# Kernel tuning notes

Measured on AMD Instinct MI355X. Metric: run time of the kernel, lower is better.

## Reference

```python
import jax, jax.numpy as jnp
import numpy as np

# JetBlock dims
B, T, HID = 2, 2048, 2048
H, DK, DV = 16, 128, 128
W = 4                      # dynamic short-conv kernel size
GEN_IN = 2 * H * DK        # kernel generator conditioned on concat(q, k)
GEN_HID = H * DV
EPS_NORM = 1e-6
EPS_L2 = 1e-12


def _silu(x):
    return x * jax.nn.sigmoid(x)


def setup_inputs() -> dict:
    key = jax.random.key(0)
    ks = jax.random.split(key, 12)
    s = 0.02
    return {
        "x": jax.random.normal(ks[0], (B, T, HID), jnp.float32),
        "Wq": jax.random.normal(ks[1], (HID, H * DK), jnp.float32) * s,
        "Wk": jax.random.normal(ks[2], (HID, H * DK), jnp.float32) * s,
        "Wv": jax.random.normal(ks[3], (HID, H * DV), jnp.float32) * s,
        "Wb": jax.random.normal(ks[4], (HID, H), jnp.float32) * s,
        "Wa": jax.random.normal(ks[5], (HID, H), jnp.float32) * s,
        "dt_bias": jax.random.normal(ks[6], (H,), jnp.float32) * s,
        "A_log": jax.random.normal(ks[7], (H,), jnp.float32) * 0.5,
        "gen_w1": jax.random.normal(ks[8], (GEN_IN, GEN_HID), jnp.float32) * s,
        "gen_w2": jax.random.normal(ks[9], (GEN_HID, H * DV * W), jnp.float32) * s,
        "gen_b2": jnp.zeros((H * DV * W,), jnp.float32),
        "norm_weight": jnp.ones((DV,), jnp.float32),
        "Wg": jax.random.normal(ks[10], (HID, H * DV), jnp.float32) * s,
        "Wo": jax.random.normal(ks[11], (H * DV, HID), jnp.float32) * s,
    }


def reference(x, Wq, Wk, Wv, Wb, Wa, dt_bias, A_log, gen_w1, gen_w2, gen_b2,
              norm_weight, Wg, Wo):
    # projections
    q = (x @ Wq).reshape(B, T, H, DK)
    k = (x @ Wk).reshape(B, T, H, DK)
    v = x @ Wv  # [B, T, H*DV]

    # dynamic short convolution on v, kernels generated from concat(q, k)
    gi = jnp.concatenate([q.reshape(B, T, -1), k.reshape(B, T, -1)], axis=-1)
    kern = (_silu(gi @ gen_w1) @ gen_w2 + gen_b2).reshape(B, T, H * DV, W)
    vp = jnp.pad(v, ((0, 0), (W - 1, 0), (0, 0)))  # causal left pad
    # out[t, d] = sum_w kern[t, d, w] * v[t - (W-1) + w, d]
    vconv = kern[..., 0] * vp[:, 0:T, :]
    for w in range(1, W):
        vconv = vconv + kern[..., w] * vp[:, w:w + T, :]
    v = _silu(vconv).reshape(B, T, H, DV)

    # gating params (gated-deltanet parameterization)
    beta = jax.nn.sigmoid(x @ Wb)                              # [B, T, H]
    g = -jnp.exp(A_log) * jax.nn.softplus(x @ Wa + dt_bias)    # log-space decay <= 0
    decay = jnp.exp(g)

    # qk l2 norm (F.normalize semantics)
    qn = q / jnp.maximum(jnp.linalg.norm(q, axis=-1, keepdims=True), EPS_L2)
    kn = k / jnp.maximum(jnp.linalg.norm(k, axis=-1, keepdims=True), EPS_L2)

    # gated delta rule recurrence (o_t reads state BEFORE the update, per source)
    def step(S, inps):
        q_t, k_t, v_t, g_t, b_t = inps
        o_t = jnp.einsum('bnkv,bnk->bnv', S, q_t)
        Sk = jnp.einsum('bnkv,bnk->bnv', S, k_t)
        delta = v_t - Sk
        S = g_t[..., None, None] * S + b_t[..., None, None] * (
            k_t[..., :, None] * delta[..., None, :])
        return S, o_t

    S0 = jnp.zeros((B, H, DK, DV), x.dtype)
    xs = (jnp.moveaxis(qn, 1, 0), jnp.moveaxis(kn, 1, 0), jnp.moveaxis(v, 1, 0),
          jnp.moveaxis(decay, 1, 0), jnp.moveaxis(beta, 1, 0))
    _, o = jax.lax.scan(step, S0, xs)           # o: [T, B, H, DV]
    o = jnp.moveaxis(o, 0, 1)                   # [B, T, H, DV]

    # gated RMSNorm per head, then output projection
    gate = (x @ Wg).reshape(B, T, H, DV)
    rms = o * jax.lax.rsqrt(jnp.mean(o * o, axis=-1, keepdims=True) + EPS_NORM)
    o = rms * norm_weight * _silu(gate)
    return o.reshape(B, T, H * DV) @ Wo
```

## Files before the change

kernel.cpp:

```cpp
#include <hip/hip_runtime.h>
#include <hip/hip_bf16.h>


typedef _Float16 v8h __attribute__((ext_vector_type(8)));
typedef _Float16 v4h __attribute__((ext_vector_type(4)));
typedef _Float16 v2h __attribute__((ext_vector_type(2)));
typedef float    v4f __attribute__((ext_vector_type(4)));

__device__ __forceinline__ void gload16(const void* g, void* l) {
  __builtin_amdgcn_global_load_lds(
      (const __attribute__((address_space(1))) unsigned int*)g,
      (__attribute__((address_space(3))) unsigned int*)l, 16, 0, 0);
}

__global__ __launch_bounds__(256)
void transpose_cast(const float* __restrict__ src, _Float16* __restrict__ dst,
                    int R, int C)
{
  __shared__ float tile[32][33];
  int c0 = blockIdx.x * 32, r0 = blockIdx.y * 32;
  int tx = threadIdx.x & 31, ty = threadIdx.x >> 5;
  #pragma unroll
  for (int i = 0; i < 32; i += 8)
    tile[ty + i][tx] = src[(size_t)(r0 + ty + i) * C + c0 + tx];
  __syncthreads();
  #pragma unroll
  for (int i = 0; i < 32; i += 8)
    dst[(size_t)(c0 + ty + i) * R + r0 + tx] = (_Float16)tile[tx][ty + i];
}

__global__ __launch_bounds__(256)
void cast_f32_f16(const float* __restrict__ src, _Float16* __restrict__ dst, int n4)
{
  int i = blockIdx.x * 256 + threadIdx.x;
  if (i >= n4) return;
  float4 v = ((const float4*)src)[i];
  v4h h = {(_Float16)v.x, (_Float16)v.y, (_Float16)v.z, (_Float16)v.w};
  *(v4h*)&dst[4 * (size_t)i] = h;
}

template<int MODE>
__global__ __launch_bounds__(512, 2)
void gemm256(const _Float16* __restrict__ A, const _Float16* __restrict__ Bt,
             void* __restrict__ Cout, const float* __restrict__ bias,
             int M, int N, int K)
{
  __shared__ _Float16 lds[65536];
  const int tid  = threadIdx.x;
  const int lane = tid & 63;
  const int wid  = tid >> 6;
  const int wm   = wid >> 2;
  const int wn   = wid & 3;
  const int l16  = lane & 15;
  const int q8   = (lane >> 4) * 8;
  const int swzx = (l16 & 7) << 3;

  const int nbx = N >> 8;
  const int cpx = gridDim.x >> 3;
  const int swz = (blockIdx.x & 7) * cpx + (blockIdx.x >> 3);
  const int bm0 = (swz / nbx) << 8;
  const int bn0 = (swz % nbx) << 8;

  const _Float16* Abase = A  + (size_t)bm0 * K;
  const _Float16* Bbase = Bt + (size_t)bn0 * K;

  const int r0 = tid >> 3;
  const int cs = ((tid & 7) * 8) ^ ((r0 & 7) << 3);

#define SLOTA(par, half) (lds + ((par) * 2 + (half)) * 8192)
#define SLOTB(par, half) (lds + 32768 + ((par) * 2 + (half)) * 8192)
#define STAGE(basep, kt, slot) do {                                        \
    _Float16* sst_ = (slot);                                               \
    gload16((basep) + (size_t)r0 * K + (kt) + cs, sst_ + tid * 8);         \
    gload16((basep) + (size_t)(r0 + 64) * K + (kt) + cs,                   \
            sst_ + 4096 + tid * 8);                                        \
  } while (0)
#define LOADA(par, mh) do {                                                \
    const _Float16* sld_ = SLOTA(par, mh);                                 \
    _Pragma("unroll")                                                      \
    for (int ks = 0; ks < 2; ks++)                                         \
      _Pragma("unroll")                                                    \
      for (int mi = 0; mi < 4; mi++)                                       \
        af[ks][mi] = *(const v8h*)&sld_[(wm * 64 + mi * 16 + l16) * 64 +   \
                                        ((ks * 32 + q8) ^ swzx)];          \
  } while (0)
#define LOADB(par, nh) do {                                                \
    const _Float16* sld_ = SLOTB(par, nh);                                 \
    _Pragma("unroll")                                                      \
    for (int ks = 0; ks < 2; ks++)                                         \
      _Pragma("unroll")                                                    \
      for (int ni = 0; ni < 2; ni++)                                       \
        bf[ks][ni] = *(const v8h*)&sld_[(wn * 32 + ni * 16 + l16) * 64 +   \
                                        ((ks * 32 + q8) ^ swzx)];          \
  } while (0)
#define MMAC(mh, nh) do {                                                  \
    __builtin_amdgcn_s_setprio(1);                                         \
    _Pragma("unroll")                                                      \
    for (int ks = 0; ks < 2; ks++)                                         \
      _Pragma("unroll")                                                    \
      for (int mi = 0; mi < 4; mi++)                                       \
        _Pragma("unroll")                                                  \
        for (int ni = 0; ni < 2; ni++)                                     \
          acc[mh][mi][nh][ni] = __builtin_amdgcn_mfma_f32_16x16x32_f16(    \
              af[ks][mi], bf[ks][ni], acc[mh][mi][nh][ni], 0, 0, 0);       \
    __builtin_amdgcn_s_setprio(0);                                         \
  } while (0)

  v4f acc[2][4][2][2];
  #pragma unroll
  for (int mh = 0; mh < 2; mh++)
    #pragma unroll
    for (int mi = 0; mi < 4; mi++)
      #pragma unroll
      for (int nh = 0; nh < 2; nh++)
        #pragma unroll
        for (int ni = 0; ni < 2; ni++)
          acc[mh][mi][nh][ni] = v4f{0.f, 0.f, 0.f, 0.f};
  v8h af[2][4], bf[2][2];

  const int nt = K >> 6;

  STAGE(Abase,                   0,  SLOTA(0, 0));
  STAGE(Bbase,                   0,  SLOTB(0, 0));
  STAGE(Abase + (size_t)128 * K, 0,  SLOTA(0, 1));
  STAGE(Bbase + (size_t)128 * K, 0,  SLOTB(0, 1));
  STAGE(Abase,                   64, SLOTA(1, 0));
  STAGE(Bbase + (size_t)128 * K, 64, SLOTB(1, 1));
  asm volatile("s_waitcnt vmcnt(4)" ::: "memory");
  __builtin_amdgcn_s_barrier();

  for (int T = 0; T < nt; T++) {
    const int par = T & 1;
    const int kt1 = (T + 1) << 6;
    const int kt2 = (T + 2) << 6;
    LOADA(par, 0);
    LOADB(par, 0);
    if (T + 1 < nt) STAGE(Abase + (size_t)128 * K, kt1, SLOTA(par ^ 1, 1));
    __builtin_amdgcn_s_barrier();
    MMAC(0, 0);
    __builtin_amdgcn_s_barrier();
    LOADB(par, 1);
    if (T + 1 < nt) STAGE(Bbase, kt1, SLOTB(par ^ 1, 0));
    __builtin_amdgcn_s_barrier();
    MMAC(0, 1);
    __builtin_amdgcn_s_barrier();
    LOADA(par, 1);
    if (T + 2 < nt) STAGE(Abase, kt2, SLOTA(par, 0));
    __builtin_amdgcn_s_barrier();
    MMAC(1, 1);
    __builtin_amdgcn_s_barrier();
    LOADB(par, 0);
    if (T + 2 < nt) STAGE(Bbase + (size_t)128 * K, kt2, SLOTB(par, 1));
    __builtin_amdgcn_s_barrier();
    MMAC(1, 0);
    if (T + 2 < nt) { asm volatile("s_waitcnt vmcnt(4)" ::: "memory"); }
    else            { asm volatile("s_waitcnt vmcnt(0)" ::: "memory"); }
    __builtin_amdgcn_s_barrier();
  }

  const int q4 = (lane >> 4) * 4;
  #pragma unroll
  for (int mh = 0; mh < 2; mh++) {
    #pragma unroll
    for (int mi = 0; mi < 4; mi++) {
      #pragma unroll
      for (int nh = 0; nh < 2; nh++) {
        #pragma unroll
        for (int ni = 0; ni < 2; ni++) {
          const int gn = bn0 + nh * 128 + wn * 32 + ni * 16 + l16;
          #pragma unroll
          for (int r = 0; r < 4; r++) {
            const int gm = bm0 + mh * 128 + wm * 64 + mi * 16 + q4 + r;
            float val = acc[mh][mi][nh][ni][r];
            size_t offc = (size_t)gm * N + gn;
            if (MODE == 0) {
              ((float*)Cout)[offc] = val;
            } else if (MODE == 1) {
              float s = val / (1.0f + expf(-val));
              ((_Float16*)Cout)[offc] = (_Float16)s;
            } else if (MODE == 2) {
              float s = val + bias[gn];
              ((_Float16*)Cout)[offc] = (_Float16)s;
            } else {
              ((_Float16*)Cout)[offc] = (_Float16)val;
            }
          }
        }
      }
    }
  }
#undef SLOTA
#undef SLOTB
#undef STAGE
#undef LOADA
#undef LOADB
#undef MMAC
}

__global__ __launch_bounds__(256)
void conv_silu(const _Float16* __restrict__ vg, const _Float16* __restrict__ kernc,
               float* __restrict__ vprime, int chunk)
{
  int idx = blockIdx.x * 256 + threadIdx.x;
  int btl = idx >> 11;
  int d   = idx & 2047;
  int btg = chunk * 2048 + btl;
  v4h kv = *(const v4h*)&kernc[(size_t)btl * 8192 + d * 4];
  float kw0 = (float)kv[0], kw1 = (float)kv[1], kw2 = (float)kv[2], kw3 = (float)kv[3];
  const _Float16* vcol = vg + d;
  float acc = kw3 * (float)vcol[(size_t)btg * 4096];
  if (btl >= 1) acc += kw2 * (float)vcol[(size_t)(btg - 1) * 4096];
  if (btl >= 2) acc += kw1 * (float)vcol[(size_t)(btg - 2) * 4096];
  if (btl >= 3) acc += kw0 * (float)vcol[(size_t)(btg - 3) * 4096];
  vprime[(size_t)btg * 2048 + d] = acc / (1.0f + expf(-acc));
}

__global__ __launch_bounds__(256)
void beta_decay(const float* __restrict__ x, const float* __restrict__ Wb,
                const float* __restrict__ Wa, const float* __restrict__ dt_bias,
                const float* __restrict__ A_log,
                float* __restrict__ beta, float* __restrict__ glog)
{
  __shared__ float xs[2048];
  __shared__ float red[8][32];
  int row = blockIdx.x;
  int tid = threadIdx.x;
  for (int i = tid; i < 2048; i += 256) xs[i] = x[(size_t)row * 2048 + i];
  __syncthreads();
  int j = tid & 31, kg = tid >> 5;
  const float* W = (j < 16) ? Wb : Wa;
  int jj = j & 15;
  float acc = 0.f;
  int k0 = kg * 256;
  for (int k = k0; k < k0 + 256; k++) acc += xs[k] * W[(size_t)k * 16 + jj];
  red[kg][j] = acc;
  __syncthreads();
  if (tid < 32) {
    float s = 0.f;
    #pragma unroll
    for (int g2 = 0; g2 < 8; g2++) s += red[g2][tid];
    int hh = tid & 15;
    if (tid < 16) {
      beta[(size_t)row * 16 + hh] = 1.0f / (1.0f + expf(-s));
    } else {
      float tt = s + dt_bias[hh];
      float sp = (tt > 20.f) ? tt : log1pf(expf(tt));
      glog[(size_t)row * 16 + hh] = -expf(A_log[hh]) * sp;
    }
  }
}

__global__ __launch_bounds__(256)
void recurrence_chunked(const _Float16* __restrict__ gi,
                        const float* __restrict__ vprime,
                        const float* __restrict__ betab,
                        const float* __restrict__ glogb,
                        float* __restrict__ o)
{
  __shared__ _Float16 Q16[32][136];
  __shared__ _Float16 K16[32][136];
  __shared__ _Float16 KT16[2][128][40];
  __shared__ _Float16 St16[64][136];
  __shared__ float V32[32][68];
  __shared__ float W0L[32][65];
  __shared__ float O0L[32][65];
  __shared__ float At32[32][32];
  __shared__ _Float16 B16[32][40];
  __shared__ _Float16 Ut16[64][40];
  __shared__ _Float16 Utp16[64][40];
  __shared__ float lgA[2][32], lgm1A[2][32], gm1E[2][32], bGA[2][32],
                   psA[2][32], betA[2][32], p31A[2];

  const int tid  = threadIdx.x;
  const int wid  = tid >> 6;
  const int lane = tid & 63;
  const int l16  = lane & 15;
  const int q8   = (lane >> 4) * 8;
  const int q4   = (lane >> 4) * 4;
  const int rg   = lane >> 4;
  const int wc   = wid * 16 + l16;

  const int blk = blockIdx.x;
  const int dvh = blk & 1;
  const int h   = (blk >> 1) & 15;
  const int b   = blk >> 5;

  const _Float16* gq = gi + (size_t)b * 2048 * 4096 + h * 128;
  const _Float16* gk = gq + 2048;
  const float* vsrc = vprime + (size_t)b * 2048 * 2048 + h * 128 + dvh * 64;
  float* ob = o + ((size_t)b * 2048 * 16 + h) * 128 + dvh * 64;

  const int sr  = tid >> 3;
  const int sc8 = tid & 7;
  const int c0  = sc8 * 16;

  v4f sfr[8];
  #pragma unroll
  for (int tn = 0; tn < 8; tn++) sfr[tn] = v4f{0.f, 0.f, 0.f, 0.f};

  v8h pq0, pq1, pk0, pk1;
  float4 pv0, pv1;
  float pg = 0.f, pb = 0.f;

  auto stage_regs = [&](int t0) {
    pq0 = *(const v8h*)(gq + (size_t)(t0 + sr) * 4096 + c0);
    pq1 = *(const v8h*)(gq + (size_t)(t0 + sr) * 4096 + c0 + 8);
    pk0 = *(const v8h*)(gk + (size_t)(t0 + sr) * 4096 + c0);
    pk1 = *(const v8h*)(gk + (size_t)(t0 + sr) * 4096 + c0 + 8);
    pv0 = *(const float4*)(vsrc + (size_t)(t0 + sr) * 2048 + sc8 * 8);
    pv1 = *(const float4*)(vsrc + (size_t)(t0 + sr) * 2048 + sc8 * 8 + 4);
    if (tid < 32) {
      size_t bt_ = (size_t)(b * 2048 + t0 + tid) * 16 + h;
      pg = glogb[bt_];
      pb = betab[bt_];
    }
  };

  auto write_stage = [&](int pn) {
    float qf[16], kf[16];
    #pragma unroll
    for (int m = 0; m < 8; m++) {
      qf[m] = (float)pq0[m]; qf[m + 8] = (float)pq1[m];
      kf[m] = (float)pk0[m]; kf[m + 8] = (float)pk1[m];
    }
    float ssq = 0.f, ssk = 0.f;
    #pragma unroll
    for (int m = 0; m < 16; m++) { ssq += qf[m] * qf[m]; ssk += kf[m] * kf[m]; }
    ssq += __shfl_xor(ssq, 1); ssq += __shfl_xor(ssq, 2); ssq += __shfl_xor(ssq, 4);
    ssk += __shfl_xor(ssk, 1); ssk += __shfl_xor(ssk, 2); ssk += __shfl_xor(ssk, 4);
    float iq = 1.0f / fmaxf(sqrtf(ssq), 1e-12f);
    float ik = 1.0f / fmaxf(sqrtf(ssk), 1e-12f);
    v8h qo0, qo1, ko0, ko1;
    #pragma unroll
    for (int m = 0; m < 8; m++) {
      qo0[m] = (_Float16)(qf[m] * iq); qo1[m] = (_Float16)(qf[m + 8] * iq);
      ko0[m] = (_Float16)(kf[m] * ik); ko1[m] = (_Float16)(kf[m + 8] * ik);
    }
    *(v8h*)&Q16[sr][c0]     = qo0;
    *(v8h*)&Q16[sr][c0 + 8] = qo1;
    *(v8h*)&K16[sr][c0]     = ko0;
    *(v8h*)&K16[sr][c0 + 8] = ko1;
    #pragma unroll
    for (int m = 0; m < 8; m++) {
      KT16[pn][c0 + m][sr]     = ko0[m];
      KT16[pn][c0 + 8 + m][sr] = ko1[m];
    }
    *(float4*)&V32[sr][sc8 * 8]     = pv0;
    *(float4*)&V32[sr][sc8 * 8 + 4] = pv1;
    if (tid < 32) {
      float s = pg;
      #pragma unroll
      for (int d = 1; d < 32; d <<= 1) {
        float t = __shfl_up(s, d, 64);
        if (lane >= d) s += t;
      }
      float lg31 = __shfl(s, 31, 64);
      float lgm1 = s - pg;
      lgA[pn][lane]   = s;
      lgm1A[pn][lane] = lgm1;
      float g1 = expf(lgm1);
      gm1E[pn][lane]  = g1;
      bGA[pn][lane]   = pb * g1;
      psA[pn][lane]   = expf(lg31 - s);
      betA[pn][lane]  = pb;
      if (lane == 0) p31A[pn] = expf(lg31);
    }
  };

  stage_regs(0);
  for (int i = tid; i < 64 * 136; i += 256) (&St16[0][0])[i] = (_Float16)0.f;
  write_stage(0);
  __syncthreads();

  const v4f zf = {0.f, 0.f, 0.f, 0.f};

  for (int c = 0; c < 64; c++) {
    const int par = c & 1;

    if (c < 63) { stage_regs((c + 1) * 32); __builtin_amdgcn_sched_barrier(0); }

    v4f kkf = zf, qkf = zf, w0f0 = zf, w0f1 = zf, o0f0 = zf, o0f1 = zf;
    {
      const int ai = (wid >> 1) * 16 + l16;
      const int bj = (wid & 1) * 16 + l16;
      #pragma unroll
      for (int ks = 0; ks < 4; ks++) {
        const int ko = ks * 32 + q8;
        v8h bs  = *(const v8h*)&St16[wid * 16 + l16][ko];
        v8h ak0 = *(const v8h*)&K16[l16][ko];
        v8h ak1 = *(const v8h*)&K16[16 + l16][ko];
        v8h aq0 = *(const v8h*)&Q16[l16][ko];
        v8h aq1 = *(const v8h*)&Q16[16 + l16][ko];
        w0f0 = __builtin_amdgcn_mfma_f32_16x16x32_f16(ak0, bs, w0f0, 0, 0, 0);
        w0f1 = __builtin_amdgcn_mfma_f32_16x16x32_f16(ak1, bs, w0f1, 0, 0, 0);
        o0f0 = __builtin_amdgcn_mfma_f32_16x16x32_f16(aq0, bs, o0f0, 0, 0, 0);
        o0f1 = __builtin_amdgcn_mfma_f32_16x16x32_f16(aq1, bs, o0f1, 0, 0, 0);
        v8h akk = *(const v8h*)&K16[ai][ko];
        v8h aqq = *(const v8h*)&Q16[ai][ko];
        v8h bkk = *(const v8h*)&K16[bj][ko];
        kkf = __builtin_amdgcn_mfma_f32_16x16x32_f16(akk, bkk, kkf, 0, 0, 0);
        qkf = __builtin_amdgcn_mfma_f32_16x16x32_f16(aqq, bkk, qkf, 0, 0, 0);
      }
    }
    {
      const int i0 = (wid >> 1) * 16, j = (wid & 1) * 16 + l16;
      #pragma unroll
      for (int fr = 0; fr < 4; fr++) {
        const int i = i0 + q4 + fr;
        float ex = expf(fminf(lgm1A[par][i] - lgA[par][j], 0.f));
        const bool lt = (j < i);
        At32[j][i] = lt ? betA[par][i] * ex * kkf[fr] : 0.f;
        B16[i][j]  = lt ? (_Float16)(ex * qkf[fr]) : (_Float16)0.f;
      }
      #pragma unroll
      for (int fr = 0; fr < 4; fr++) {
        W0L[q4 + fr][wid * 16 + l16]      = w0f0[fr];
        W0L[16 + q4 + fr][wid * 16 + l16] = w0f1[fr];
        O0L[q4 + fr][wid * 16 + l16]      = o0f0[fr];
        O0L[16 + q4 + fr][wid * 16 + l16] = o0f1[fr];
      }
    }
    __syncthreads();

    float ru[8];
    #pragma unroll
    for (int jj = 0; jj < 8; jj++) {
      const int row = rg * 8 + jj;
      ru[jj] = betA[par][row] * V32[row][wc] - bGA[par][row] * W0L[row][wc];
    }
    #pragma unroll
    for (int j = 0; j < 32; j++) {
      float uj = __shfl(ru[j & 7], (j >> 3) * 16 + l16, 64);
      const v4f a0 = *(const v4f*)&At32[j][rg * 8];
      const v4f a1 = *(const v4f*)&At32[j][rg * 8 + 4];
      ru[0] -= a0[0] * uj; ru[1] -= a0[1] * uj;
      ru[2] -= a0[2] * uj; ru[3] -= a0[3] * uj;
      ru[4] -= a1[0] * uj; ru[5] -= a1[1] * uj;
      ru[6] -= a1[2] * uj; ru[7] -= a1[3] * uj;
    }
    {
      v8h uo, upo;
      #pragma unroll
      for (int jj = 0; jj < 8; jj++) {
        uo[jj]  = (_Float16)ru[jj];
        upo[jj] = (_Float16)(ru[jj] * psA[par][rg * 8 + jj]);
      }
      *(v8h*)&Ut16[wc][rg * 8]  = uo;
      *(v8h*)&Utp16[wc][rg * 8] = upo;
    }
    __syncthreads();

    {
      v8h bu = *(const v8h*)&Ut16[wid * 16 + l16][q8];
      #pragma unroll
      for (int t2i = 0; t2i < 2; t2i++) {
        v8h a = *(const v8h*)&B16[t2i * 16 + l16][q8];
        v4f d = __builtin_amdgcn_mfma_f32_16x16x32_f16(a, bu, zf, 0, 0, 0);
        #pragma unroll
        for (int fr = 0; fr < 4; fr++) {
          const int i = t2i * 16 + q4 + fr;
          const int cc = wid * 16 + l16;
          ob[(size_t)(c * 32 + i) * 2048 + cc] =
              gm1E[par][i] * O0L[i][cc] + d[fr];
        }
      }
      const float p31 = p31A[par];
      v8h ua = *(const v8h*)&Utp16[wid * 16 + l16][q8];
      #pragma unroll
      for (int tn = 0; tn < 8; tn++) {
        v8h bk = *(const v8h*)&KT16[par][tn * 16 + l16][q8];
        v4f sc = {sfr[tn][0] * p31, sfr[tn][1] * p31,
                  sfr[tn][2] * p31, sfr[tn][3] * p31};
        sfr[tn] = __builtin_amdgcn_mfma_f32_16x16x32_f16(ua, bk, sc, 0, 0, 0);
        #pragma unroll
        for (int fr = 0; fr < 4; fr++)
          St16[wid * 16 + q4 + fr][tn * 16 + l16] = (_Float16)sfr[tn][fr];
      }
    }
    if (c < 63) write_stage((c + 1) & 1);
    __syncthreads();
  }
}

__global__ __launch_bounds__(256)
void rms_gate(const float* __restrict__ o, const _Float16* __restrict__ vg,
              const float* __restrict__ normw, _Float16* __restrict__ yh)
{
  int task = blockIdx.x * 4 + (threadIdx.x >> 6);
  int lane = threadIdx.x & 63;
  int bt = task >> 4, h = task & 15;
  float2 v = *(const float2*)(o + (size_t)task * 128 + lane * 2);
  float ss = v.x * v.x + v.y * v.y;
  #pragma unroll
  for (int m = 1; m < 64; m <<= 1) ss += __shfl_xor(ss, m);
  float r = rsqrtf(ss * (1.0f / 128.0f) + 1e-6f);
  v2h gt2 = *(const v2h*)(vg + (size_t)bt * 4096 + 2048 + h * 128 + lane * 2);
  float gx = (float)gt2[0], gy = (float)gt2[1];
  float2 nw = *(const float2*)(normw + lane * 2);
  float g0 = gx / (1.0f + expf(-gx));
  float g1 = gy / (1.0f + expf(-gy));
  v2h outp = {(_Float16)(v.x * r * nw.x * g0), (_Float16)(v.y * r * nw.y * g1)};
  *(v2h*)(yh + (size_t)bt * 2048 + h * 128 + lane * 2) = outp;
}

extern "C" void kernel_launch(void* const* d_in, const int* in_sizes, int n_in,
                              void* d_out, int out_size, void* d_ws, size_t ws_size,
                              hipStream_t stream)
{
  (void)in_sizes; (void)n_in; (void)out_size;
  const float* x       = (const float*)d_in[0];
  const float* Wq      = (const float*)d_in[1];
  const float* Wk      = (const float*)d_in[2];
  const float* Wv      = (const float*)d_in[3];
  const float* Wb      = (const float*)d_in[4];
  const float* Wa      = (const float*)d_in[5];
  const float* dt_bias = (const float*)d_in[6];
  const float* A_log   = (const float*)d_in[7];
  const float* gen_w1  = (const float*)d_in[8];
  const float* gen_w2  = (const float*)d_in[9];
  const float* gen_b2  = (const float*)d_in[10];
  const float* normw   = (const float*)d_in[11];
  const float* Wg      = (const float*)d_in[12];
  const float* Wo      = (const float*)d_in[13];

  const size_t SZ_GI   = 4096ull * 4096 * 2;
  const size_t SZ_VG   = 4096ull * 4096 * 2;
  const size_t SZ_WT   = 8192ull * 2048 * 2;
  const size_t SZ_D    = 4096ull * 2048 * 2;
  const size_t SZ_KC   = 2048ull * 8192 * 2;
  const size_t SZ_VP   = 4096ull * 2048 * 4;
  const size_t SZ_SM   = 4096ull * 16 * 4;
  const size_t NEEDED = SZ_GI + SZ_VG + SZ_WT + SZ_D + SZ_KC + SZ_VP + 2 * SZ_SM;
  if (ws_size < NEEDED) return;

  char* w = (char*)d_ws;
  _Float16* gi     = (_Float16*)(w);
  _Float16* vg     = (_Float16*)(w + SZ_GI);
  _Float16* Wt     = (_Float16*)(w + SZ_GI + SZ_VG);
  char*     Dreg   =            (w + SZ_GI + SZ_VG + SZ_WT);
  _Float16* kernc  = (_Float16*)(w + SZ_GI + SZ_VG + SZ_WT + SZ_D);
  float*    vprime = (float*)   (w + SZ_GI + SZ_VG + SZ_WT + SZ_D + SZ_KC);
  float*    betab  = (float*)   (w + SZ_GI + SZ_VG + SZ_WT + SZ_D + SZ_KC + SZ_VP);
  float*    glogb  = (float*)   (w + SZ_GI + SZ_VG + SZ_WT + SZ_D + SZ_KC + SZ_VP + SZ_SM);
  _Float16* xh  = (_Float16*)Dreg;
  _Float16* hid = (_Float16*)Dreg;
  _Float16* yh  = (_Float16*)Dreg;
  float* obuf = (float*)d_out;

  dim3 blk(256);
  dim3 blk512(512);

  cast_f32_f16<<<8192, blk, 0, stream>>>(x, xh, 4096 * 2048 / 4);

  transpose_cast<<<dim3(64, 64), blk, 0, stream>>>(Wq, Wt, 2048, 2048);
  transpose_cast<<<dim3(64, 64), blk, 0, stream>>>(Wk, Wt + 2048 * 2048, 2048, 2048);
  gemm256<3><<<256, blk512, 0, stream>>>(xh, Wt, gi, nullptr, 4096, 4096, 2048);

  transpose_cast<<<dim3(64, 64), blk, 0, stream>>>(Wv, Wt, 2048, 2048);
  transpose_cast<<<dim3(64, 64), blk, 0, stream>>>(Wg, Wt + 2048 * 2048, 2048, 2048);
  gemm256<3><<<256, blk512, 0, stream>>>(xh, Wt, vg, nullptr, 4096, 4096, 2048);

  transpose_cast<<<dim3(64, 128), blk, 0, stream>>>(gen_w1, Wt, 4096, 2048);
  gemm256<1><<<128, blk512, 0, stream>>>(gi, Wt, hid, nullptr, 4096, 2048, 4096);

  transpose_cast<<<dim3(256, 64), blk, 0, stream>>>(gen_w2, Wt, 2048, 8192);
  for (int chunk = 0; chunk < 2; chunk++) {
    gemm256<2><<<256, blk512, 0, stream>>>(hid + (size_t)chunk * 2048 * 2048, Wt,
                                           kernc, gen_b2, 2048, 8192, 2048);
    conv_silu<<<16384, blk, 0, stream>>>(vg, kernc, vprime, chunk);
  }

  beta_decay<<<4096, blk, 0, stream>>>(x, Wb, Wa, dt_bias, A_log, betab, glogb);
  recurrence_chunked<<<64, blk, 0, stream>>>(gi, vprime, betab, glogb, obuf);
  rms_gate<<<16384, blk, 0, stream>>>(obuf, vg, normw, yh);

  transpose_cast<<<dim3(64, 64), blk, 0, stream>>>(Wo, Wt, 2048, 2048);
  gemm256<0><<<128, blk512, 0, stream>>>(yh, Wt, (float*)d_out, nullptr, 4096, 2048, 2048);
}
```

Before: 1.102 ms.

## Split delta-rule recurrence into two time segments with basis-state propagation

The recurrence over 2048 steps is split into two halves that run concurrently. One set of blocks processes the first half and writes its end state. A second set processes the second half from zero state. A third set runs the second half with an identity initial state to build a basis for how the output depends on the initial state. A new apply_basis kernel multiplies that basis by the first half's end state and adds the correction to the second-half outputs. This triples the block count from 64 to 192 to fill more of the GPU and halves the serial chain length, at the cost of extra work, fp16 rounding in the basis path, and an extra kernel. It also XOR-swizzles the KT16 shared-memory layout to reduce bank conflicts.

```diff
diff --git a/kernel.cpp b/kernel.cpp
--- a/kernel.cpp
+++ b/kernel.cpp
@@ -251,11 +251,13 @@
 }
 
 __global__ __launch_bounds__(256)
-void recurrence_chunked(const _Float16* __restrict__ gi,
-                        const float* __restrict__ vprime,
-                        const float* __restrict__ betab,
-                        const float* __restrict__ glogb,
-                        float* __restrict__ o)
+void recurrence_seg(const _Float16* __restrict__ gi,
+                    const float* __restrict__ vprime,
+                    const float* __restrict__ betab,
+                    const float* __restrict__ glogb,
+                    float* __restrict__ o,
+                    float* __restrict__ Send,
+                    _Float16* __restrict__ obasis)
 {
   __shared__ _Float16 Q16[32][136];
   __shared__ _Float16 K16[32][136];
@@ -280,26 +282,36 @@
   const int rg   = lane >> 4;
   const int wc   = wid * 16 + l16;
 
-  const int blk = blockIdx.x;
-  const int dvh = blk & 1;
-  const int h   = (blk >> 1) & 15;
-  const int b   = blk >> 5;
+  const int role = blockIdx.x >> 6;
+  const int blk  = blockIdx.x & 63;
+  const int dvh  = blk & 1;
+  const int h    = (blk >> 1) & 15;
+  const int b    = blk >> 5;
+  const int tbase = (role == 0) ? 0 : 1024;
+  const bool basis = (role == 2);
 
   const _Float16* gq = gi + (size_t)b * 2048 * 4096 + h * 128;
   const _Float16* gk = gq + 2048;
   const float* vsrc = vprime + (size_t)b * 2048 * 2048 + h * 128 + dvh * 64;
-  float* ob = o + ((size_t)b * 2048 * 16 + h) * 128 + dvh * 64;
+  float* ob = o + ((size_t)(b * 2048 + tbase) * 16 + h) * 128 + dvh * 64;
+  _Float16* obb = obasis + ((size_t)b * 1024 * 16 + h) * 128 + dvh * 64;
 
   const int sr  = tid >> 3;
   const int sc8 = tid & 7;
   const int c0  = sc8 * 16;
+  const int ktsw = (tid & 3) << 3;
 
   v4f sfr[8];
   #pragma unroll
-  for (int tn = 0; tn < 8; tn++) sfr[tn] = v4f{0.f, 0.f, 0.f, 0.f};
+  for (int tn = 0; tn < 8; tn++) {
+    #pragma unroll
+    for (int fr = 0; fr < 4; fr++)
+      sfr[tn][fr] = (basis && (tn * 16 + l16) == (dvh * 64 + wid * 16 + q4 + fr))
+                        ? 1.f : 0.f;
+  }
 
   v8h pq0, pq1, pk0, pk1;
-  float4 pv0, pv1;
+  float4 pv0 = {0.f, 0.f, 0.f, 0.f}, pv1 = {0.f, 0.f, 0.f, 0.f};
   float pg = 0.f, pb = 0.f;
 
   auto stage_regs = [&](int t0) {
@@ -307,8 +319,10 @@
     pq1 = *(const v8h*)(gq + (size_t)(t0 + sr) * 4096 + c0 + 8);
     pk0 = *(const v8h*)(gk + (size_t)(t0 + sr) * 4096 + c0);
     pk1 = *(const v8h*)(gk + (size_t)(t0 + sr) * 4096 + c0 + 8);
-    pv0 = *(const float4*)(vsrc + (size_t)(t0 + sr) * 2048 + sc8 * 8);
-    pv1 = *(const float4*)(vsrc + (size_t)(t0 + sr) * 2048 + sc8 * 8 + 4);
+    if (!basis) {
+      pv0 = *(const float4*)(vsrc + (size_t)(t0 + sr) * 2048 + sc8 * 8);
+      pv1 = *(const float4*)(vsrc + (size_t)(t0 + sr) * 2048 + sc8 * 8 + 4);
+    }
     if (tid < 32) {
       size_t bt_ = (size_t)(b * 2048 + t0 + tid) * 16 + h;
       pg = glogb[bt_];
@@ -342,8 +356,8 @@
     *(v8h*)&K16[sr][c0 + 8] = ko1;
     #pragma unroll
     for (int m = 0; m < 8; m++) {
-      KT16[pn][c0 + m][sr]     = ko0[m];
-      KT16[pn][c0 + 8 + m][sr] = ko1[m];
+      KT16[pn][c0 + m][sr ^ ktsw]     = ko0[m];
+      KT16[pn][c0 + 8 + m][sr ^ ktsw] = ko1[m];
     }
     *(float4*)&V32[sr][sc8 * 8]     = pv0;
     *(float4*)&V32[sr][sc8 * 8 + 4] = pv1;
@@ -367,17 +381,21 @@
     }
   };
 
-  stage_regs(0);
-  for (int i = tid; i < 64 * 136; i += 256) (&St16[0][0])[i] = (_Float16)0.f;
+  stage_regs(tbase);
+  for (int i = tid; i < 64 * 136; i += 256) {
+    int r_ = i / 136, cc_ = i - r_ * 136;
+    (&St16[0][0])[i] =
+        (basis && cc_ == dvh * 64 + r_) ? (_Float16)1.f : (_Float16)0.f;
+  }
   write_stage(0);
   __syncthreads();
 
   const v4f zf = {0.f, 0.f, 0.f, 0.f};
 
-  for (int c = 0; c < 64; c++) {
+  for (int c = 0; c < 32; c++) {
     const int par = c & 1;
 
-    if (c < 63) { stage_regs((c + 1) * 32); __builtin_amdgcn_sched_barrier(0); }
+    if (c < 31) { stage_regs(tbase + (c + 1) * 32); __builtin_amdgcn_sched_barrier(0); }
 
     v4f kkf = zf, qkf = zf, w0f0 = zf, w0f1 = zf, o0f0 = zf, o0f1 = zf;
     {
@@ -460,15 +478,17 @@
         for (int fr = 0; fr < 4; fr++) {
           const int i = t2i * 16 + q4 + fr;
           const int cc = wid * 16 + l16;
-          ob[(size_t)(c * 32 + i) * 2048 + cc] =
-              gm1E[par][i] * O0L[i][cc] + d[fr];
+          float val = gm1E[par][i] * O0L[i][cc] + d[fr];
+          size_t off = (size_t)(c * 32 + i) * 2048 + cc;
+          if (basis) obb[off] = (_Float16)val;
+          else       ob[off] = val;
         }
       }
       const float p31 = p31A[par];
       v8h ua = *(const v8h*)&Utp16[wid * 16 + l16][q8];
       #pragma unroll
       for (int tn = 0; tn < 8; tn++) {
-        v8h bk = *(const v8h*)&KT16[par][tn * 16 + l16][q8];
+        v8h bk = *(const v8h*)&KT16[par][tn * 16 + l16][q8 ^ ((tn & 3) << 3)];
         v4f sc = {sfr[tn][0] * p31, sfr[tn][1] * p31,
                   sfr[tn][2] * p31, sfr[tn][3] * p31};
         sfr[tn] = __builtin_amdgcn_mfma_f32_16x16x32_f16(ua, bk, sc, 0, 0, 0);
@@ -477,8 +497,78 @@
           St16[wid * 16 + q4 + fr][tn * 16 + l16] = (_Float16)sfr[tn][fr];
       }
     }
-    if (c < 63) write_stage((c + 1) & 1);
+    if (c < 31) write_stage((c + 1) & 1);
     __syncthreads();
+  }
+
+  if (role == 0) {
+    float* sg = Send + (size_t)(b * 16 + h) * 128 * 128;
+    #pragma unroll
+    for (int tn = 0; tn < 8; tn++)
+      #pragma unroll
+      for (int fr = 0; fr < 4; fr++)
+        sg[(size_t)(dvh * 64 + wid * 16 + q4 + fr) * 128 + tn * 16 + l16] =
+            sfr[tn][fr];
+  }
+}
+
+__global__ __launch_bounds__(256)
+void apply_basis(const _Float16* __restrict__ obasis,
+                 const float* __restrict__ Send,
+                 float* __restrict__ o)
+{
+  __shared__ _Float16 Ao[128][136];
+  __shared__ _Float16 Bs[128][136];
+  const int bh = blockIdx.x & 31;
+  const int tt = blockIdx.x >> 5;
+  const int b = bh >> 4, h = bh & 15;
+  const int tid = threadIdx.x;
+  const int wid = tid >> 6, lane = tid & 63;
+  const int l16 = lane & 15, q8 = (lane >> 4) * 8, q4 = (lane >> 4) * 4;
+
+  const _Float16* asrc = obasis + ((size_t)(b * 1024 + tt * 128) * 16 + h) * 128;
+  for (int i = tid; i < 128 * 16; i += 256) {
+    int r = i >> 4, c8 = (i & 15) * 8;
+    *(v8h*)&Ao[r][c8] = *(const v8h*)(asrc + (size_t)r * 2048 + c8);
+  }
+  const float* ssrc = Send + (size_t)bh * 128 * 128;
+  for (int i = tid; i < 128 * 16; i += 256) {
+    int r = i >> 4, c8 = (i & 15) * 8;
+    v8h tmp;
+    #pragma unroll
+    for (int m = 0; m < 8; m++) tmp[m] = (_Float16)ssrc[(size_t)r * 128 + c8 + m];
+    *(v8h*)&Bs[r][c8] = tmp;
+  }
+  __syncthreads();
+
+  v4f acc[2][8];
+  #pragma unroll
+  for (int rt = 0; rt < 2; rt++)
+    #pragma unroll
+    for (int ct = 0; ct < 8; ct++) acc[rt][ct] = v4f{0.f, 0.f, 0.f, 0.f};
+  #pragma unroll
+  for (int ks = 0; ks < 4; ks++) {
+    v8h af0 = *(const v8h*)&Ao[wid * 32 + l16][ks * 32 + q8];
+    v8h af1 = *(const v8h*)&Ao[wid * 32 + 16 + l16][ks * 32 + q8];
+    #pragma unroll
+    for (int ct = 0; ct < 8; ct++) {
+      v8h bf = *(const v8h*)&Bs[ct * 16 + l16][ks * 32 + q8];
+      acc[0][ct] = __builtin_amdgcn_mfma_f32_16x16x32_f16(af0, bf, acc[0][ct], 0, 0, 0);
+      acc[1][ct] = __builtin_amdgcn_mfma_f32_16x16x32_f16(af1, bf, acc[1][ct], 0, 0, 0);
+    }
+  }
+  float* obp = o + ((size_t)(b * 2048 + 1024 + tt * 128) * 16 + h) * 128;
+  #pragma unroll
+  for (int rt = 0; rt < 2; rt++) {
+    #pragma unroll
+    for (int ct = 0; ct < 8; ct++) {
+      #pragma unroll
+      for (int fr = 0; fr < 4; fr++) {
+        const int row = wid * 32 + rt * 16 + q4 + fr;
+        const int col = ct * 16 + l16;
+        obp[(size_t)row * 2048 + col] += acc[rt][ct][fr];
+      }
+    }
   }
 }
 
@@ -547,6 +637,9 @@
   _Float16* yh  = (_Float16*)Dreg;
   float* obuf = (float*)d_out;
 
+  _Float16* obasis = (_Float16*)(w + SZ_GI + SZ_VG);
+  float*    Send   = (float*)   (w + SZ_GI + SZ_VG + 2ull * 1024 * 16 * 128 * 2);
+
   dim3 blk(256);
   dim3 blk512(512);
 
@@ -571,7 +664,9 @@
   }
 
   beta_decay<<<4096, blk, 0, stream>>>(x, Wb, Wa, dt_bias, A_log, betab, glogb);
-  recurrence_chunked<<<64, blk, 0, stream>>>(gi, vprime, betab, glogb, obuf);
+  recurrence_seg<<<192, blk, 0, stream>>>(gi, vprime, betab, glogb, obuf,
+                                          Send, obasis);
+  apply_basis<<<256, blk, 0, stream>>>(obasis, Send, obuf);
   rms_gate<<<16384, blk, 0, stream>>>(obuf, vg, normw, yh);
 
   transpose_cast<<<dim3(64, 64), blk, 0, stream>>>(Wo, Wt, 2048, 2048);
```

Result: faster. 968.9 us (-12.1%).
